# Kernel optimization log

Hardware: AMD Instinct MI355X
Metric: run time of the kernel (lower is better)

## Reference

```python
import jax, jax.numpy as jnp
import numpy as np

TOPK = 6
ROUTE_SCALE = 1.5


def setup_inputs() -> dict:
    key = jax.random.key(0)
    k1, k2, k3 = jax.random.split(key, 3)
    N, D, E = 16384, 4096, 256
    x = jax.random.normal(k1, (N, D), dtype=jnp.float32)
    weight = jax.random.normal(k2, (E, D), dtype=jnp.float32) * (D ** -0.5)
    bias = jax.random.normal(k3, (E,), dtype=jnp.float32) * 0.02
    return {"x": x, "weight": weight, "bias": bias}


def reference(x, weight, bias):
    # gate linear: [N, D] @ [E, D]^T -> [N, E], computed in fp32
    scores = jnp.einsum('nd,ed->ne', x.astype(jnp.float32), weight.astype(jnp.float32))
    # sqrtsoftplus score function
    original_scores = jnp.sqrt(jax.nn.softplus(scores))
    # bias only affects expert selection, not the routing weights
    biased = original_scores + bias
    _, indices = jax.lax.top_k(biased, TOPK)          # [N, TOPK] int32
    weights = jnp.take_along_axis(original_scores, indices, axis=-1)
    # non-softmax score func -> renormalize selected weights
    weights = weights / jnp.sum(weights, axis=-1, keepdims=True)
    weights = weights * ROUTE_SCALE
    return weights, indices
```

## Files before the change

kernel.cpp:

```cpp
#include <hip/hip_runtime.h>
#include <math.h>

constexpr int D     = 4096;
constexpr int D2    = 2048;
constexpr int D4    = 1024;
constexpr int E     = 256;
constexpr int TK    = 6;
constexpr int BM    = 64;
constexpr int NT    = 1024;
constexpr int NTILE = 128;
constexpr float TAU = 3e-5f;

typedef __attribute__((ext_vector_type(8)))  short short8;
typedef __attribute__((ext_vector_type(16))) float float16;
typedef unsigned short ushort_t;

#define GAS __attribute__((address_space(1)))
#define LAS __attribute__((address_space(3)))

__device__ __forceinline__ ushort_t f2bf(float f) {
  unsigned u = __float_as_uint(f);
  return (ushort_t)((u + 0x7fffu + ((u >> 16) & 1u)) >> 16);
}
__device__ __forceinline__ float bf2f(ushort_t h) {
  return __uint_as_float(((unsigned)h) << 16);
}
__device__ __forceinline__ int swz4(int r) { return (r & 3) ^ ((r >> 2) & 3); }

__device__ __forceinline__ void gload_lds16(const ushort_t* g, ushort_t* l) {
  __builtin_amdgcn_global_load_lds((const GAS unsigned int*)g,
                                   (LAS unsigned int*)l, 16, 0, 0);
}

struct __align__(16) SMem {
  union {
    struct {
      ushort_t Bh[4][8][32 * 32];
      ushort_t Bl[4][8][32 * 32];
      ushort_t Ah[2][BM * 32];
      ushort_t Al[2][BM * 32];
    } st;
    struct {
      float red[8][2][16][64];
      float val[BM * 65];
      int   id [BM * 65];
    } ep;
  } u;
  float  bias[E];
  int    nflag;
  int    flagrow[BM];
  int    flagid[BM][8];
  double exact[8];
};
static_assert(sizeof(SMem) <= 160 * 1024, "LDS overflow");

__global__ __launch_bounds__(256)
void conv_w(const float* __restrict__ wg, ushort_t* __restrict__ whi,
            ushort_t* __restrict__ wlo)
{
  size_t i = (size_t)blockIdx.x * 256 + threadIdx.x;
  float4 v = ((const float4*)wg)[i];
  float a[4] = {v.x, v.y, v.z, v.w};
  ushort_t h[4], l[4];
#pragma unroll
  for (int j = 0; j < 4; ++j) {
    h[j] = f2bf(a[j]);
    l[j] = f2bf(a[j] - bf2f(h[j]));
  }
  *(uint2*)&whi[i * 4] = *(uint2*)h;
  *(uint2*)&wlo[i * 4] = *(uint2*)l;
}

#define WAITV3   asm volatile("s_waitcnt vmcnt(3)" ::: "memory")
#define WAITV2   asm volatile("s_waitcnt vmcnt(2)" ::: "memory")
#define WAITV0   asm volatile("s_waitcnt vmcnt(0)" ::: "memory")
#define LGKM0    asm volatile("s_waitcnt lgkmcnt(0)" ::: "memory")
#define MEMFENCE asm volatile("" ::: "memory")

__global__ __launch_bounds__(NT, 4)
void gate_kernel(const float* __restrict__ xg, const float* __restrict__ wg,
                 const float* __restrict__ bg,
                 const ushort_t* __restrict__ whi, const ushort_t* __restrict__ wlo,
                 float* __restrict__ outw, float* __restrict__ outi)
{
  __shared__ SMem sm;
  const int t    = threadIdx.x;
  const int row0 = blockIdx.x * BM;
  const int wv   = t >> 6;
  const int lane = t & 63;
  const int m    = lane & 31;
  const int hf   = lane >> 5;
  const int eg   = wv >> 1;
  const int kh   = wv & 1;

  if (t < E) sm.bias[t] = bg[t];
  if (t == 0) sm.nflag = 0;

  const float2* x2 = (const float2*)xg;
  const float4* x4 = (const float4*)xg;
  const float4* w4 = (const float4*)wg;

  float16 acc0, acc1;
#pragma unroll
  for (int i = 0; i < 16; ++i) { acc0[i] = 0.f; acc1[i] = 0.f; }

  const int a_row = t >> 4;
  const int aq    = t & 15;

  const int e16 = lane >> 2;
  const int ch  = lane & 3;

  const int sA = swz4(m);
  const int slR = ((2 * kh + hf) ^ sA) * 8;

  const ushort_t* wsrc = kh ? wlo : whi;

  auto stage_B = [&](int kt, int p) {
    ushort_t* dstbase = kh ? &sm.u.st.Bl[p][eg][0] : &sm.u.st.Bh[p][eg][0];
#pragma unroll
    for (int j = 0; j < 2; ++j) {
      const int er = j * 16 + e16;
      const int cs = ch ^ swz4(er);
      const size_t go = (size_t)(eg * 32 + er) * D + kt * 32 + cs * 8;
      gload_lds16(wsrc + go, dstbase + j * 512);
    }
  };
  auto ldx = [&](int kt) {
    return x2[(size_t)(row0 + a_row) * D2 + kt * 16 + aq];
  };
  auto store_A = [&](int p, float2 xv) {
    ushort_t h0 = f2bf(xv.x), h1 = f2bf(xv.y);
    ushort_t l0 = f2bf(xv.x - bf2f(h0)), l1 = f2bf(xv.y - bf2f(h1));
    const int c = aq >> 2, sub = aq & 3;
    const int sl = ((c ^ swz4(a_row)) << 3) + sub * 2;
    unsigned hp = (unsigned)h0 | ((unsigned)h1 << 16);
    unsigned lp = (unsigned)l0 | ((unsigned)l1 << 16);
    *(unsigned*)&sm.u.st.Ah[p][a_row * 32 + sl] = hp;
    *(unsigned*)&sm.u.st.Al[p][a_row * 32 + sl] = lp;
  };
  auto compute = [&](int pa, int pb) {
    short8 a0h = *(const short8*)&sm.u.st.Ah[pa][m * 32 + slR];
    short8 a0l = *(const short8*)&sm.u.st.Al[pa][m * 32 + slR];
    short8 a1h = *(const short8*)&sm.u.st.Ah[pa][(32 + m) * 32 + slR];
    short8 a1l = *(const short8*)&sm.u.st.Al[pa][(32 + m) * 32 + slR];
    short8 bh  = *(const short8*)&sm.u.st.Bh[pb][eg][m * 32 + slR];
    short8 bl  = *(const short8*)&sm.u.st.Bl[pb][eg][m * 32 + slR];
    acc0 = __builtin_amdgcn_mfma_f32_32x32x16_bf16(a0h, bh, acc0, 0, 0, 0);
    acc0 = __builtin_amdgcn_mfma_f32_32x32x16_bf16(a0h, bl, acc0, 0, 0, 0);
    acc0 = __builtin_amdgcn_mfma_f32_32x32x16_bf16(a0l, bh, acc0, 0, 0, 0);
    acc1 = __builtin_amdgcn_mfma_f32_32x32x16_bf16(a1h, bh, acc1, 0, 0, 0);
    acc1 = __builtin_amdgcn_mfma_f32_32x32x16_bf16(a1h, bl, acc1, 0, 0, 0);
    acc1 = __builtin_amdgcn_mfma_f32_32x32x16_bf16(a1l, bh, acc1, 0, 0, 0);
  };

  stage_B(0, 0);
  stage_B(1, 1);
  float2 x0v = ldx(0);
  float2 xA  = ldx(1);
  float2 xB  = ldx(2);
  WAITV2;
  store_A(0, x0v);
  LGKM0;
  __builtin_amdgcn_s_barrier();
  MEMFENCE;

#define TILE_BODY(KT, XS)                                                     \
  do {                                                                        \
    store_A(((KT) + 1) & 1, XS);                                              \
    { const int kl = ((KT) + 3 < NTILE) ? (KT) + 3 : NTILE - 1;               \
      XS = ldx(kl); }                                                         \
    { const int kb = ((KT) + 2 < NTILE) ? (KT) + 2 : NTILE - 1;               \
      stage_B(kb, ((KT) + 2) & 3); }                                          \
    compute((KT) & 1, (KT) & 3);                                              \
    WAITV3;                                      \
    LGKM0;                                              \
    __builtin_amdgcn_s_barrier();                                             \
    MEMFENCE;                                                                 \
  } while (0)

  for (int it = 0; it < NTILE / 4; ++it) {
    const int kt = it * 4;
    TILE_BODY(kt + 0, xA);
    TILE_BODY(kt + 1, xB);
    TILE_BODY(kt + 2, xA);
    TILE_BODY(kt + 3, xB);
  }
#undef TILE_BODY

  WAITV0;
  __syncthreads();

  if (kh == 1) {
#pragma unroll
    for (int r = 0; r < 16; ++r) {
      sm.u.ep.red[eg][0][r][lane] = acc0[r];
      sm.u.ep.red[eg][1][r][lane] = acc1[r];
    }
  }
  __syncthreads();
  if (kh == 0) {
#pragma unroll
    for (int r = 0; r < 16; ++r) {
      acc0[r] += sm.u.ep.red[eg][0][r][lane];
      acc1[r] += sm.u.ep.red[eg][1][r][lane];
    }
  }

  const int myE = eg * 32 + m;
  const float myBias = sm.bias[myE];

  if (kh == 0) {
#pragma unroll
    for (int b = 0; b < 2; ++b) {
#pragma unroll
      for (int reg = 0; reg < 16; ++reg) {
        const int row_local = b * 32 + (reg & 3) + 8 * (reg >> 2) + 4 * hf;
        float s = b ? acc1[reg] : acc0[reg];
        float v = sqrtf(fmaxf(s, 0.f) + log1pf(expf(-fabsf(s)))) + myBias;
#pragma unroll
        for (int ssel = 0; ssel < 8; ++ssel) {
          float bv = v;
#pragma unroll
          for (int off = 1; off < 32; off <<= 1)
            bv = fmaxf(bv, __shfl_xor(bv, off, 64));
          unsigned long long ball = __ballot(v == bv);
          unsigned hm = (unsigned)(ball >> (hf * 32));
          int mwin = __ffs(hm) - 1;
          if (m == mwin) {
            sm.u.ep.val[row_local * 65 + eg * 8 + ssel] = v;
            sm.u.ep.id [row_local * 65 + eg * 8 + ssel] = myE;
            v = -INFINITY;
          }
        }
      }
    }
  }
  __syncthreads();

  if (t < 512) {
    const int r = t >> 3, g = t & 7;
    float mv[8]; int mi[8];
#pragma unroll
    for (int q = 0; q < 8; ++q) {
      mv[q] = sm.u.ep.val[r * 65 + q * 8 + g];
      mi[q] = sm.u.ep.id [r * 65 + q * 8 + g];
    }
    float tv[8]; int ti[8];
#pragma unroll
    for (int s = 0; s < 8; ++s) {
      float bv = mv[0]; int bi = mi[0];
#pragma unroll
      for (int q = 1; q < 8; ++q)
        if (mv[q] > bv || (mv[q] == bv && mi[q] < bi)) { bv = mv[q]; bi = mi[q]; }
#pragma unroll
      for (int off = 1; off < 8; off <<= 1) {
        float ov = __shfl_xor(bv, off, 64);
        int   oi = __shfl_xor(bi, off, 64);
        if (ov > bv || (ov == bv && oi < bi)) { bv = ov; bi = oi; }
      }
      tv[s] = bv; ti[s] = bi;
#pragma unroll
      for (int q = 0; q < 8; ++q)
        if (mi[q] == bi) mv[q] = -INFINITY;
    }
    if (g == 0) {
      bool flag = false;
#pragma unroll
      for (int i = 0; i < 7; ++i) flag |= (tv[i] - tv[i + 1] < TAU);
      const int grow = row0 + r;
      if (!flag) {
        float og[6], ssum = 0.f;
#pragma unroll
        for (int i = 0; i < 6; ++i) { og[i] = tv[i] - sm.bias[ti[i]]; ssum += og[i]; }
        const float sc = 1.5f / ssum;
#pragma unroll
        for (int i = 0; i < 6; ++i) {
          outw[(size_t)grow * TK + i] = og[i] * sc;
          outi[(size_t)grow * TK + i] = (float)ti[i];
        }
      } else {
        int slot = atomicAdd(&sm.nflag, 1);
        sm.flagrow[slot] = grow;
#pragma unroll
        for (int i = 0; i < 8; ++i) sm.flagid[slot][i] = ti[i];
      }
    }
  }
  __syncthreads();

  const int nf = sm.nflag;
  for (int f = 0; f < nf; ++f) {
    const int grow = sm.flagrow[f];
    if (wv < 8) {
      const int e = sm.flagid[f][wv];
      double accd = 0.0;
      const float4* xr = x4 + (size_t)grow * D4 + lane * 16;
      const float4* wr = w4 + (size_t)e    * D4 + lane * 16;
#pragma unroll
      for (int i = 0; i < 16; ++i) {
        float4 xv = xr[i], wl = wr[i];
        accd = fma((double)xv.x, (double)wl.x, accd);
        accd = fma((double)xv.y, (double)wl.y, accd);
        accd = fma((double)xv.z, (double)wl.z, accd);
        accd = fma((double)xv.w, (double)wl.w, accd);
      }
#pragma unroll
      for (int off = 1; off < 64; off <<= 1)
        accd += __shfl_xor(accd, off, 64);
      if (lane == 0) {
        double sp = fmax(accd, 0.0) + log1p(exp(-fabs(accd)));
        sm.exact[wv] = sqrt(sp);
      }
    }
    __syncthreads();
    if (t == 0) {
      double ov[8]; int oid[8], ordr[8];
      for (int i = 0; i < 8; ++i) { ov[i] = sm.exact[i]; oid[i] = sm.flagid[f][i]; ordr[i] = i; }
      for (int i = 0; i < 6; ++i) {
        int b = i;
        for (int j = i + 1; j < 8; ++j) {
          double bj = ov[ordr[j]] + (double)sm.bias[oid[ordr[j]]];
          double bb = ov[ordr[b]] + (double)sm.bias[oid[ordr[b]]];
          if (bj > bb || (bj == bb && oid[ordr[j]] < oid[ordr[b]])) b = j;
        }
        int tmp = ordr[i]; ordr[i] = ordr[b]; ordr[b] = tmp;
      }
      double ssum = 0.0;
      for (int i = 0; i < 6; ++i) ssum += ov[ordr[i]];
      double sc = 1.5 / ssum;
      for (int i = 0; i < 6; ++i) {
        outw[(size_t)grow * TK + i] = (float)(ov[ordr[i]] * sc);
        outi[(size_t)grow * TK + i] = (float)oid[ordr[i]];
      }
    }
    __syncthreads();
  }
}

extern "C" void kernel_launch(void* const* d_in, const int* in_sizes, int n_in,
                              void* d_out, int out_size, void* d_ws, size_t ws_size,
                              hipStream_t stream) {
  const float* x = (const float*)d_in[0];
  const float* w = (const float*)d_in[1];
  const float* b = (const float*)d_in[2];
  float* out  = (float*)d_out;
  const int N = in_sizes[0] / D;

  ushort_t* whi = (ushort_t*)d_ws;
  ushort_t* wlo = whi + (size_t)E * D;

  float* outw = out;
  float* outi = out + (size_t)N * TK;

  hipLaunchKernelGGL(conv_w, dim3(E * D / 4 / 256), dim3(256), 0, stream,
                     w, whi, wlo);
  hipLaunchKernelGGL(gate_kernel, dim3(N / BM), dim3(NT), 0, stream,
                     x, w, b, whi, wlo, outw, outi);
}
```

Baseline: 586.4 us.

## Load B fragments directly from retiled global weights; stage A in large chunks

Result: faster. 552.7 us (-5.8%).

```diff
diff --git a/kernel.cpp b/kernel.cpp
--- a/kernel.cpp
+++ b/kernel.cpp
@@ -2,22 +2,20 @@
 #include <math.h>
 
 constexpr int D     = 4096;
-constexpr int D2    = 2048;
 constexpr int D4    = 1024;
 constexpr int E     = 256;
 constexpr int TK    = 6;
 constexpr int BM    = 64;
 constexpr int NT    = 1024;
-constexpr int NTILE = 128;
+constexpr int CK    = 512;
+constexpr int NCH   = D / CK;
+constexpr int NST   = CK / 32;
 constexpr float TAU = 3e-5f;
 
 typedef __attribute__((ext_vector_type(8)))  short short8;
 typedef __attribute__((ext_vector_type(16))) float float16;
 typedef unsigned short ushort_t;
 
-#define GAS __attribute__((address_space(1)))
-#define LAS __attribute__((address_space(3)))
-
 __device__ __forceinline__ ushort_t f2bf(float f) {
   unsigned u = __float_as_uint(f);
   return (ushort_t)((u + 0x7fffu + ((u >> 16) & 1u)) >> 16);
@@ -25,20 +23,11 @@
 __device__ __forceinline__ float bf2f(ushort_t h) {
   return __uint_as_float(((unsigned)h) << 16);
 }
-__device__ __forceinline__ int swz4(int r) { return (r & 3) ^ ((r >> 2) & 3); }
-
-__device__ __forceinline__ void gload_lds16(const ushort_t* g, ushort_t* l) {
-  __builtin_amdgcn_global_load_lds((const GAS unsigned int*)g,
-                                   (LAS unsigned int*)l, 16, 0, 0);
-}
 
 struct __align__(16) SMem {
   union {
     struct {
-      ushort_t Bh[4][8][32 * 32];
-      ushort_t Bl[4][8][32 * 32];
-      ushort_t Ah[2][BM * 32];
-      ushort_t Al[2][BM * 32];
+      ushort_t A2[BM * 1024];
     } st;
     struct {
       float red[8][2][16][64];
@@ -59,6 +48,10 @@
             ushort_t* __restrict__ wlo)
 {
   size_t i = (size_t)blockIdx.x * 256 + threadIdx.x;
+  const int e  = (int)(i >> 10);
+  const int k4 = (int)(i & 1023);
+  const int kt = k4 >> 3;
+  const int kw = (k4 & 7) * 4;
   float4 v = ((const float4*)wg)[i];
   float a[4] = {v.x, v.y, v.z, v.w};
   ushort_t h[4], l[4];
@@ -67,15 +60,10 @@
     h[j] = f2bf(a[j]);
     l[j] = f2bf(a[j] - bf2f(h[j]));
   }
-  *(uint2*)&whi[i * 4] = *(uint2*)h;
-  *(uint2*)&wlo[i * 4] = *(uint2*)l;
-}
-
-#define WAITV3   asm volatile("s_waitcnt vmcnt(3)" ::: "memory")
-#define WAITV2   asm volatile("s_waitcnt vmcnt(2)" ::: "memory")
-#define WAITV0   asm volatile("s_waitcnt vmcnt(0)" ::: "memory")
-#define LGKM0    asm volatile("s_waitcnt lgkmcnt(0)" ::: "memory")
-#define MEMFENCE asm volatile("" ::: "memory")
+  const size_t dst = (size_t)kt * (E * 32) + e * 32 + kw;
+  *(uint2*)&whi[dst] = *(uint2*)h;
+  *(uint2*)&wlo[dst] = *(uint2*)l;
+}
 
 __global__ __launch_bounds__(NT, 4)
 void gate_kernel(const float* __restrict__ xg, const float* __restrict__ wg,
@@ -96,7 +84,6 @@
   if (t < E) sm.bias[t] = bg[t];
   if (t == 0) sm.nflag = 0;
 
-  const float2* x2 = (const float2*)xg;
   const float4* x4 = (const float4*)xg;
   const float4* w4 = (const float4*)wg;
 
@@ -105,89 +92,60 @@
   for (int i = 0; i < 16; ++i) { acc0[i] = 0.f; acc1[i] = 0.f; }
 
   const int a_row = t >> 4;
-  const int aq    = t & 15;
-
-  const int e16 = lane >> 2;
-  const int ch  = lane & 3;
-
-  const int sA = swz4(m);
-  const int slR = ((2 * kh + hf) ^ sA) * 8;
-
-  const ushort_t* wsrc = kh ? wlo : whi;
-
-  auto stage_B = [&](int kt, int p) {
-    ushort_t* dstbase = kh ? &sm.u.st.Bl[p][eg][0] : &sm.u.st.Bh[p][eg][0];
-#pragma unroll
-    for (int j = 0; j < 2; ++j) {
-      const int er = j * 16 + e16;
-      const int cs = ch ^ swz4(er);
-      const size_t go = (size_t)(eg * 32 + er) * D + kt * 32 + cs * 8;
-      gload_lds16(wsrc + go, dstbase + j * 512);
+  const int kc    = t & 15;
+
+  const int q  = kh * 2 + hf;
+  const int b2 = (m >> 2) & 1;
+  const ushort_t* a0P = &sm.u.st.A2[m        * 1024 + ((q ^ (m & 3)) << 3)];
+  const ushort_t* a1P = &sm.u.st.A2[(32 + m) * 1024 + ((q ^ (m & 3)) << 3)];
+
+  const size_t bOff = (size_t)(eg * 32 + m) * 32 + kh * 16 + hf * 8;
+
+  auto stage_A = [&](int c) {
+    const float4* src = x4 + (size_t)(row0 + a_row) * D4 + c * 128 + kc;
+#pragma unroll
+    for (int j = 0; j < 8; ++j) {
+      float4 v = src[j * 16];
+      float a[4] = {v.x, v.y, v.z, v.w};
+      ushort_t h[4], l[4];
+#pragma unroll
+      for (int i = 0; i < 4; ++i) {
+        h[i] = f2bf(a[i]);
+        l[i] = f2bf(a[i] - bf2f(h[i]));
+      }
+      const int slot = j * 8 + (kc >> 1);
+      const int half = kc & 1;
+      const int sw   = ((slot ^ (a_row & 7)) << 3) + half * 4;
+      *(uint2*)&sm.u.st.A2[a_row * 1024 + sw]       = *(uint2*)h;
+      *(uint2*)&sm.u.st.A2[a_row * 1024 + 512 + sw] = *(uint2*)l;
     }
   };
-  auto ldx = [&](int kt) {
-    return x2[(size_t)(row0 + a_row) * D2 + kt * 16 + aq];
-  };
-  auto store_A = [&](int p, float2 xv) {
-    ushort_t h0 = f2bf(xv.x), h1 = f2bf(xv.y);
-    ushort_t l0 = f2bf(xv.x - bf2f(h0)), l1 = f2bf(xv.y - bf2f(h1));
-    const int c = aq >> 2, sub = aq & 3;
-    const int sl = ((c ^ swz4(a_row)) << 3) + sub * 2;
-    unsigned hp = (unsigned)h0 | ((unsigned)h1 << 16);
-    unsigned lp = (unsigned)l0 | ((unsigned)l1 << 16);
-    *(unsigned*)&sm.u.st.Ah[p][a_row * 32 + sl] = hp;
-    *(unsigned*)&sm.u.st.Al[p][a_row * 32 + sl] = lp;
-  };
-  auto compute = [&](int pa, int pb) {
-    short8 a0h = *(const short8*)&sm.u.st.Ah[pa][m * 32 + slR];
-    short8 a0l = *(const short8*)&sm.u.st.Al[pa][m * 32 + slR];
-    short8 a1h = *(const short8*)&sm.u.st.Ah[pa][(32 + m) * 32 + slR];
-    short8 a1l = *(const short8*)&sm.u.st.Al[pa][(32 + m) * 32 + slR];
-    short8 bh  = *(const short8*)&sm.u.st.Bh[pb][eg][m * 32 + slR];
-    short8 bl  = *(const short8*)&sm.u.st.Bl[pb][eg][m * 32 + slR];
-    acc0 = __builtin_amdgcn_mfma_f32_32x32x16_bf16(a0h, bh, acc0, 0, 0, 0);
-    acc0 = __builtin_amdgcn_mfma_f32_32x32x16_bf16(a0h, bl, acc0, 0, 0, 0);
-    acc0 = __builtin_amdgcn_mfma_f32_32x32x16_bf16(a0l, bh, acc0, 0, 0, 0);
-    acc1 = __builtin_amdgcn_mfma_f32_32x32x16_bf16(a1h, bh, acc1, 0, 0, 0);
-    acc1 = __builtin_amdgcn_mfma_f32_32x32x16_bf16(a1h, bl, acc1, 0, 0, 0);
-    acc1 = __builtin_amdgcn_mfma_f32_32x32x16_bf16(a1l, bh, acc1, 0, 0, 0);
-  };
-
-  stage_B(0, 0);
-  stage_B(1, 1);
-  float2 x0v = ldx(0);
-  float2 xA  = ldx(1);
-  float2 xB  = ldx(2);
-  WAITV2;
-  store_A(0, x0v);
-  LGKM0;
-  __builtin_amdgcn_s_barrier();
-  MEMFENCE;
-
-#define TILE_BODY(KT, XS)                                                     \
-  do {                                                                        \
-    store_A(((KT) + 1) & 1, XS);                                              \
-    { const int kl = ((KT) + 3 < NTILE) ? (KT) + 3 : NTILE - 1;               \
-      XS = ldx(kl); }                                                         \
-    { const int kb = ((KT) + 2 < NTILE) ? (KT) + 2 : NTILE - 1;               \
-      stage_B(kb, ((KT) + 2) & 3); }                                          \
-    compute((KT) & 1, (KT) & 3);                                              \
-    WAITV3;                                      \
-    LGKM0;                                              \
-    __builtin_amdgcn_s_barrier();                                             \
-    MEMFENCE;                                                                 \
-  } while (0)
-
-  for (int it = 0; it < NTILE / 4; ++it) {
-    const int kt = it * 4;
-    TILE_BODY(kt + 0, xA);
-    TILE_BODY(kt + 1, xB);
-    TILE_BODY(kt + 2, xA);
-    TILE_BODY(kt + 3, xB);
-  }
-#undef TILE_BODY
-
-  WAITV0;
+
+  for (int c = 0; c < NCH; ++c) {
+    __syncthreads();
+    stage_A(c);
+    __syncthreads();
+
+    const ushort_t* bH = whi + (size_t)(c * NST) * 8192 + bOff;
+    const ushort_t* bL = wlo + (size_t)(c * NST) * 8192 + bOff;
+#pragma unroll 4
+    for (int s = 0; s < NST; ++s) {
+      short8 bh = *(const short8*)(bH + (size_t)s * 8192);
+      short8 bl = *(const short8*)(bL + (size_t)s * 8192);
+      const int ao = (s ^ b2) << 5;
+      short8 a0h = *(const short8*)(a0P + ao);
+      short8 a0l = *(const short8*)(a0P + 512 + ao);
+      short8 a1h = *(const short8*)(a1P + ao);
+      short8 a1l = *(const short8*)(a1P + 512 + ao);
+      acc0 = __builtin_amdgcn_mfma_f32_32x32x16_bf16(a0h, bh, acc0, 0, 0, 0);
+      acc0 = __builtin_amdgcn_mfma_f32_32x32x16_bf16(a0h, bl, acc0, 0, 0, 0);
+      acc0 = __builtin_amdgcn_mfma_f32_32x32x16_bf16(a0l, bh, acc0, 0, 0, 0);
+      acc1 = __builtin_amdgcn_mfma_f32_32x32x16_bf16(a1h, bh, acc1, 0, 0, 0);
+      acc1 = __builtin_amdgcn_mfma_f32_32x32x16_bf16(a1h, bl, acc1, 0, 0, 0);
+      acc1 = __builtin_amdgcn_mfma_f32_32x32x16_bf16(a1l, bh, acc1, 0, 0, 0);
+    }
+  }
+
   __syncthreads();
 
   if (kh == 1) {
@@ -241,17 +199,17 @@
     const int r = t >> 3, g = t & 7;
     float mv[8]; int mi[8];
 #pragma unroll
-    for (int q = 0; q < 8; ++q) {
-      mv[q] = sm.u.ep.val[r * 65 + q * 8 + g];
-      mi[q] = sm.u.ep.id [r * 65 + q * 8 + g];
+    for (int q2 = 0; q2 < 8; ++q2) {
+      mv[q2] = sm.u.ep.val[r * 65 + q2 * 8 + g];
+      mi[q2] = sm.u.ep.id [r * 65 + q2 * 8 + g];
     }
     float tv[8]; int ti[8];
 #pragma unroll
     for (int s = 0; s < 8; ++s) {
       float bv = mv[0]; int bi = mi[0];
 #pragma unroll
-      for (int q = 1; q < 8; ++q)
-        if (mv[q] > bv || (mv[q] == bv && mi[q] < bi)) { bv = mv[q]; bi = mi[q]; }
+      for (int q2 = 1; q2 < 8; ++q2)
+        if (mv[q2] > bv || (mv[q2] == bv && mi[q2] < bi)) { bv = mv[q2]; bi = mi[q2]; }
 #pragma unroll
       for (int off = 1; off < 8; off <<= 1) {
         float ov = __shfl_xor(bv, off, 64);
@@ -260,8 +218,8 @@
       }
       tv[s] = bv; ti[s] = bi;
 #pragma unroll
-      for (int q = 0; q < 8; ++q)
-        if (mi[q] == bi) mv[q] = -INFINITY;
+      for (int q2 = 0; q2 < 8; ++q2)
+        if (mi[q2] == bi) mv[q2] = -INFINITY;
     }
     if (g == 0) {
       bool flag = false;
```
